# Kernel tuning notes

Measured on AMD Instinct MI355X. Metric: run time of the kernel, lower is better.

## Reference

```python
import jax, jax.numpy as jnp
import numpy as np

B, C, H, W = 2, 128, 64, 64


def setup_inputs() -> dict:
    key = jax.random.key(0)
    ks = jax.random.split(key, 16)
    s = 1.0 / np.sqrt(C)
    d = {
        "x": jax.random.normal(ks[0], (B, C, H, W), jnp.float32),
        "y": jax.random.normal(ks[1], (B, C, H, W), jnp.float32),
    }
    names = ["qr", "qi", "kr", "ki", "vr", "vi"]
    for i, n in enumerate(names):
        d["W" + n] = jax.random.normal(ks[2 + 2 * i], (C, C), jnp.float32) * s
        d["b" + n] = jax.random.normal(ks[3 + 2 * i], (C,), jnp.float32) * s
    return d


def _lin(t, Wt, bt):
    # t: [b, n, c]; torch Linear: t @ W^T + b
    return jnp.einsum("bnc,dc->bnd", t, Wt) + bt


def reference(x, y, Wqr, bqr, Wqi, bqi, Wkr, bkr, Wki, bki, Wvr, bvr, Wvi, bvi):
    b, c, h, w = x.shape
    xf = jnp.fft.fft2(x)  # over last two axes (h, w)
    yf = jnp.fft.fft2(y)
    # b c h w -> b (h w) c
    def flat(t):
        return t.transpose(0, 2, 3, 1).reshape(b, h * w, c)
    xr, xi = flat(xf.real), flat(xf.imag)
    yr, yi = flat(yf.real), flat(yf.imag)

    Qr = _lin(xr, Wqr, bqr) - _lin(xi, Wqi, bqi)
    Qi = _lin(xi, Wqr, bqr) + _lin(xr, Wqi, bqi)
    Kr = _lin(yr, Wkr, bkr) - _lin(yi, Wki, bki)
    Ki = _lin(yi, Wkr, bkr) + _lin(yr, Wki, bki)
    Vr = _lin(yr, Wvr, bvr) - _lin(yi, Wvi, bvi)
    Vi = _lin(yi, Wvr, bvr) + _lin(yr, Wvi, bvi)

    sr = jnp.einsum("bnc,bmc->bnm", Qr, Kr) - jnp.einsum("bnc,bmc->bnm", Qi, Ki)
    si = jnp.einsum("bnc,bmc->bnm", Qr, Ki) + jnp.einsum("bnc,bmc->bnm", Qi, Kr)
    scores = jnp.sqrt(sr * sr + si * si + 1e-8)
    attn = jax.nn.softmax(scores, axis=-1)

    out_r = jnp.einsum("bnm,bmc->bnc", attn, Vr)
    out_i = jnp.einsum("bnm,bmc->bnc", attn, Vi)
    out_c = jax.lax.complex(out_r, out_i)
    # b (h w) c -> b c h w
    out_c = out_c.reshape(b, h, w, c).transpose(0, 3, 1, 2)
    return jnp.fft.ifft2(out_c).real
```

## Files before the change

kernel.cpp:

```cpp
#include <hip/hip_runtime.h>
#include <math.h>


#define PI2 6.283185307179586f

typedef __attribute__((ext_vector_type(8))) short short8;
typedef __attribute__((ext_vector_type(4))) float f32x4;

#define MFMA16(A,B,C) __builtin_amdgcn_mfma_f32_16x16x32_bf16((A),(B),(C),0,0,0)

__device__ inline unsigned short f2bf(float x){
  union{float f; unsigned int u;} a; a.f = x;
  unsigned int r = (a.u + 0x7fffu + ((a.u>>16)&1u)) >> 16;
  return (unsigned short)r;
}
__device__ inline float bf2f(unsigned short h){
  union{unsigned int u; float f;} a; a.u = ((unsigned int)h)<<16; return a.f;
}
__device__ inline short8 neg8(short8 x){
  union{short8 v; unsigned int u[4];} a; a.v = x;
  a.u[0]^=0x80008000u; a.u[1]^=0x80008000u; a.u[2]^=0x80008000u; a.u[3]^=0x80008000u;
  return a.v;
}
__device__ inline void gload_lds16(const void* g, void* lds){
  __builtin_amdgcn_global_load_lds((const __attribute__((address_space(1))) unsigned int*)g,
                                   (__attribute__((address_space(3))) unsigned int*)lds,
                                   16, 0, 0);
}

__global__ __launch_bounds__(256) void dft2_fwd_kernel(
    const float* __restrict__ x, const float* __restrict__ y,
    float* __restrict__ xr, float* __restrict__ xi,
    float* __restrict__ yr, float* __restrict__ yi)
{
  __shared__ float Xs[4096];
  __shared__ float Tr[4096], Ti[4096];
  __shared__ float twc[64], tws[64];
  int blk = blockIdx.x;
  const float* src; float *outr, *outi;
  int plane;
  if (blk < 256) { src = x; outr = xr; outi = xi; plane = blk; }
  else           { src = y; outr = yr; outi = yi; plane = blk - 256; }
  int b = plane >> 7, c = plane & 127;
  int t = threadIdx.x;
  if (t < 64) {
    float ang = -PI2 * (float)t / 64.0f;
    twc[t] = cosf(ang); tws[t] = sinf(ang);
  }
  const float* p = src + ((size_t)plane << 12);
  for (int i = t; i < 4096; i += 256) Xs[i] = p[i];
  __syncthreads();
  for (int j = 0; j < 16; j++) {
    int o = t + 256 * j; int h = o >> 6, wp = o & 63;
    float ar = 0.f, ai = 0.f;
    for (int w = 0; w < 64; w++) {
      int k = (w * wp) & 63;
      float v = Xs[h * 64 + w];
      ar = fmaf(v, twc[k], ar);
      ai = fmaf(v, tws[k], ai);
    }
    Tr[h * 64 + wp] = ar; Ti[h * 64 + wp] = ai;
  }
  __syncthreads();
  size_t ob = ((size_t)b * 4096) * 128 + c;
  for (int j = 0; j < 16; j++) {
    int o = t + 256 * j; int hp = o >> 6, wp = o & 63;
    float ar = 0.f, ai = 0.f;
    for (int h = 0; h < 64; h++) {
      int k = (h * hp) & 63;
      float cr = twc[k], ci = tws[k];
      float tr = Tr[h * 64 + wp], ti = Ti[h * 64 + wp];
      ar += tr * cr - ti * ci;
      ai += tr * ci + ti * cr;
    }
    int n = (hp << 6) + wp;
    outr[ob + (size_t)n * 128] = ar;
    outi[ob + (size_t)n * 128] = ai;
  }
}

__global__ __launch_bounds__(256) void proj_pack_kernel(
    const float* __restrict__ xr, const float* __restrict__ xi,
    const float* __restrict__ yr, const float* __restrict__ yi,
    const float* __restrict__ Wqr, const float* __restrict__ bqr,
    const float* __restrict__ Wqi, const float* __restrict__ bqi,
    const float* __restrict__ Wkr, const float* __restrict__ bkr,
    const float* __restrict__ Wki, const float* __restrict__ bki,
    const float* __restrict__ Wvr, const float* __restrict__ bvr,
    const float* __restrict__ Wvi, const float* __restrict__ bvi,
    unsigned short* __restrict__ Qpk, unsigned short* __restrict__ Kpk,
    unsigned short* __restrict__ Vpk)
{
  __shared__ float Asr[64 * 33], Asi[64 * 33], Wsr[128 * 33], Wsi[128 * 33];
  int nt = blockIdx.x, lin = blockIdx.y, b = blockIdx.z;
  const float *ar, *ai, *Wr, *Wi, *br_, *bi_;
  if (lin == 0)      { ar = xr; ai = xi; Wr = Wqr; Wi = Wqi; br_ = bqr; bi_ = bqi; }
  else if (lin == 1) { ar = yr; ai = yi; Wr = Wkr; Wi = Wki; br_ = bkr; bi_ = bki; }
  else               { ar = yr; ai = yi; Wr = Wvr; Wi = Wvi; br_ = bvr; bi_ = bvi; }
  int t = threadIdx.x; int td = t & 15, tn = t >> 4;
  int n0 = nt * 64;
  size_t abase = (size_t)b * 4096 * 128 + (size_t)n0 * 128;
  float accr[4][8] = {}, acci[4][8] = {};
  for (int kk = 0; kk < 4; kk++) {
    __syncthreads();
    for (int idx = t; idx < 64 * 32; idx += 256) {
      int r = idx >> 5, ccol = idx & 31;
      Asr[r * 33 + ccol] = ar[abase + (size_t)r * 128 + kk * 32 + ccol];
      Asi[r * 33 + ccol] = ai[abase + (size_t)r * 128 + kk * 32 + ccol];
    }
    for (int idx = t; idx < 128 * 32; idx += 256) {
      int r = idx >> 5, ccol = idx & 31;
      Wsr[r * 33 + ccol] = Wr[(size_t)r * 128 + kk * 32 + ccol];
      Wsi[r * 33 + ccol] = Wi[(size_t)r * 128 + kk * 32 + ccol];
    }
    __syncthreads();
    for (int k = 0; k < 32; k++) {
      float a_r[4], a_i[4], w_r[8], w_i[8];
      #pragma unroll
      for (int i = 0; i < 4; i++) {
        a_r[i] = Asr[(tn * 4 + i) * 33 + k];
        a_i[i] = Asi[(tn * 4 + i) * 33 + k];
      }
      #pragma unroll
      for (int jj = 0; jj < 8; jj++) {
        w_r[jj] = Wsr[(td + 16 * jj) * 33 + k];
        w_i[jj] = Wsi[(td + 16 * jj) * 33 + k];
      }
      #pragma unroll
      for (int i = 0; i < 4; i++)
        #pragma unroll
        for (int jj = 0; jj < 8; jj++) {
          accr[i][jj] += a_r[i] * w_r[jj] - a_i[i] * w_i[jj];
          acci[i][jj] += a_i[i] * w_r[jj] + a_r[i] * w_i[jj];
        }
    }
  }
  for (int jj = 0; jj < 8; jj++) {
    int d = td + 16 * jj;
    float brd = br_[d], bid = bi_[d];
    #pragma unroll
    for (int i = 0; i < 4; i++) {
      int n = n0 + tn * 4 + i;
      float cr = accr[i][jj] + (brd - bid);
      float ci = acci[i][jj] + (brd + bid);
      if (lin <= 1) {
        unsigned short rh = f2bf(cr); unsigned short rl = f2bf(cr - bf2f(rh));
        unsigned short ih = f2bf(ci); unsigned short il = f2bf(ci - bf2f(ih));
        int s = d >> 5, j = d & 7;
        int lq = ((d & 31) >> 3) * 16 + (n & 15);
        if (lin == 0) {
          int tqi = n >> 4;
          size_t base = ((size_t)((b * 256 + tqi) * 16 + s)) * 512 + (size_t)lq * 8 + j;
          Qpk[base + 0 * 2048] = rh; Qpk[base + 1 * 2048] = rl;
          Qpk[base + 2 * 2048] = ih; Qpk[base + 3 * 2048] = il;
        } else {
          int mt2 = n >> 6, tml = (n >> 4) & 3;
          size_t base = ((size_t)((b * 64 + mt2) * 64 + tml * 4 + s)) * 512 + (size_t)lq * 8 + j;
          Kpk[base + 0 * 8192] = rh; Kpk[base + 1 * 8192] = rl;
          Kpk[base + 2 * 8192] = ih; Kpk[base + 3 * 8192] = il;
        }
      } else {
        int sm = n >> 5, jv = n & 7;
        int lv = ((n & 31) >> 3) * 16 + (d & 15);
        size_t b0 = ((size_t)((b * 128 + sm) * 16 + (d >> 4))) * 512 + (size_t)lv * 8 + jv;
        size_t b1 = ((size_t)((b * 128 + sm) * 16 + ((d + 128) >> 4))) * 512 + (size_t)lv * 8 + jv;
        Vpk[b0] = f2bf(cr);
        Vpk[b1] = f2bf(ci);
      }
    }
  }
}

__global__ __launch_bounds__(256, 1) void attn_mfma_kernel(
    const short* __restrict__ Qpk, const short* __restrict__ Kpk,
    const short* __restrict__ Vpk,
    float* __restrict__ Or_, float* __restrict__ Oi_)
{
  __shared__ __align__(16) short Klds[2][32768];
  __shared__ __align__(16) short Pfrag[4 * 512];
  __shared__ float rmax[2][16][2];
  __shared__ float rsum[2][16][2];

  const int b = blockIdx.y, qt = blockIdx.x;
  const int t = threadIdx.x;
  const int w = t >> 6, l = t & 63;
  const int qg = w & 1, mh = w >> 1;
  const int g = l >> 4, c = l & 15;

  const short8* Qp8 = (const short8*)Qpk;
  const int tq = qt * 2 + qg;
  short8 Qf[4][4];
  #pragma unroll
  for (int a = 0; a < 4; a++)
    #pragma unroll
    for (int s = 0; s < 4; s++)
      Qf[a][s] = Qp8[((size_t)((b * 256 + tq) * 16 + a * 4 + s)) * 64 + l];
  short8 nQih[4], nQil[4];
  #pragma unroll
  for (int s = 0; s < 4; s++) { nQih[s] = neg8(Qf[2][s]); nQil[s] = neg8(Qf[3][s]); }

  f32x4 O[8], M, L;
  #pragma unroll
  for (int nt = 0; nt < 8; nt++) O[nt] = (f32x4){0.f, 0.f, 0.f, 0.f};
  M = (f32x4){-3e38f, -3e38f, -3e38f, -3e38f};
  L = (f32x4){0.f, 0.f, 0.f, 0.f};

  const char* Kg = (const char*)Kpk;
  {
    const char* gsrc = Kg + ((size_t)(b * 64) << 16);
    char* lb = (char*)&Klds[0][0];
    #pragma unroll
    for (int i2 = 0; i2 < 16; i2++) {
      int ch = i2 * 4 + w;
      gload_lds16(gsrc + ch * 1024 + l * 16, lb + ch * 1024);
    }
  }
  const short8* Vp8 = (const short8*)Vpk;

  for (int mt = 0; mt < 64; mt++) {
    const int cur = mt & 1;
    __syncthreads();
    if (mt + 1 < 64) {
      const char* gsrc = Kg + ((size_t)(b * 64 + mt + 1) << 16);
      char* lb = (char*)&Klds[cur ^ 1][0];
      #pragma unroll
      for (int i2 = 0; i2 < 16; i2++) {
        int ch = i2 * 4 + w;
        gload_lds16(gsrc + ch * 1024 + l * 16, lb + ch * 1024);
      }
    }
    const short8* kb8 = (const short8*)&Klds[cur][0];
    f32x4 sr[2], si[2];
    #pragma unroll
    for (int tm = 0; tm < 2; tm++) { sr[tm] = (f32x4){0,0,0,0}; si[tm] = (f32x4){0,0,0,0}; }
    #pragma unroll
    for (int s = 0; s < 4; s++) {
      #pragma unroll
      for (int tm = 0; tm < 2; tm++) {
        const int tml = 2 * mh + tm;
        short8 Brh = kb8[((0 * 4 + tml) * 4 + s) * 64 + l];
        short8 Brl = kb8[((1 * 4 + tml) * 4 + s) * 64 + l];
        short8 Bih = kb8[((2 * 4 + tml) * 4 + s) * 64 + l];
        short8 Bil = kb8[((3 * 4 + tml) * 4 + s) * 64 + l];
        sr[tm] = MFMA16(Qf[0][s], Brh, sr[tm]);
        si[tm] = MFMA16(Qf[0][s], Bih, si[tm]);
        sr[tm] = MFMA16(Qf[0][s], Brl, sr[tm]);
        si[tm] = MFMA16(Qf[0][s], Bil, si[tm]);
        sr[tm] = MFMA16(Qf[1][s], Brh, sr[tm]);
        si[tm] = MFMA16(Qf[1][s], Bih, si[tm]);
        sr[tm] = MFMA16(nQih[s], Bih, sr[tm]);
        si[tm] = MFMA16(Qf[2][s], Brh, si[tm]);
        sr[tm] = MFMA16(nQih[s], Bil, sr[tm]);
        si[tm] = MFMA16(Qf[2][s], Brl, si[tm]);
        sr[tm] = MFMA16(nQil[s], Bih, sr[tm]);
        si[tm] = MFMA16(Qf[3][s], Brh, si[tm]);
      }
    }
    f32x4 s0, s1, mx;
    #pragma unroll
    for (int r = 0; r < 4; r++) {
      s0[r] = sqrtf(sr[0][r] * sr[0][r] + si[0][r] * si[0][r] + 1e-8f);
      s1[r] = sqrtf(sr[1][r] * sr[1][r] + si[1][r] * si[1][r] + 1e-8f);
      mx[r] = fmaxf(s0[r], s1[r]);
    }
    #pragma unroll
    for (int d = 1; d < 16; d <<= 1) {
      #pragma unroll
      for (int r = 0; r < 4; r++) mx[r] = fmaxf(mx[r], __shfl_xor(mx[r], d));
    }
    if (c < 4) rmax[qg][4 * g + c][mh] = mx[c];
    __syncthreads();
    f32x4 nm, esc, p0, p1, ps;
    #pragma unroll
    for (int r = 0; r < 4; r++) {
      float v = fmaxf(rmax[qg][4 * g + r][0], rmax[qg][4 * g + r][1]);
      nm[r] = fmaxf(M[r], v);
      esc[r] = __expf(M[r] - nm[r]);
      M[r] = nm[r];
      p0[r] = __expf(s0[r] - nm[r]);
      p1[r] = __expf(s1[r] - nm[r]);
      ps[r] = p0[r] + p1[r];
    }
    #pragma unroll
    for (int d = 1; d < 16; d <<= 1) {
      #pragma unroll
      for (int r = 0; r < 4; r++) ps[r] += __shfl_xor(ps[r], d);
    }
    if (c < 4) rsum[qg][4 * g + c][mh] = ps[c];
    #pragma unroll
    for (int tm = 0; tm < 2; tm++) {
      int mm = 16 * tm + c;
      int lpb = (mm >> 3) * 16;
      int j = mm & 7;
      #pragma unroll
      for (int r = 0; r < 4; r++) {
        float p = (tm == 0) ? p0[r] : p1[r];
        Pfrag[(qg * 2 + mh) * 512 + (lpb + 4 * g + r) * 8 + j] = (short)f2bf(p);
      }
    }
    __syncthreads();
    #pragma unroll
    for (int r = 0; r < 4; r++) {
      L[r] = L[r] * esc[r] + rsum[qg][4 * g + r][0] + rsum[qg][4 * g + r][1];
      #pragma unroll
      for (int nt = 0; nt < 8; nt++) O[nt][r] *= esc[r];
    }
    #pragma unroll
    for (int ks = 0; ks < 2; ks++) {
      short8 Pa = *(const short8*)&Pfrag[(qg * 2 + ks) * 512 + l * 8];
      const size_t vb = ((size_t)((b * 128 + mt * 2 + ks) * 16 + mh * 8)) * 64 + l;
      #pragma unroll
      for (int nt = 0; nt < 8; nt++) {
        short8 Vb = Vp8[vb + (size_t)nt * 64];
        O[nt] = MFMA16(Pa, Vb, O[nt]);
      }
    }
  }
  const size_t base = (size_t)b * 4096 * 128;
  f32x4 inv;
  #pragma unroll
  for (int r = 0; r < 4; r++) inv[r] = 1.0f / L[r];
  #pragma unroll
  for (int nt = 0; nt < 8; nt++) {
    int cc = mh * 128 + nt * 16 + c;
    #pragma unroll
    for (int r = 0; r < 4; r++) {
      int row = qt * 32 + qg * 16 + 4 * g + r;
      float v = O[nt][r] * inv[r];
      if (cc < 128) Or_[base + (size_t)row * 128 + cc] = v;
      else          Oi_[base + (size_t)row * 128 + cc - 128] = v;
    }
  }
}

__global__ __launch_bounds__(256) void idft2_kernel(
    const float* __restrict__ Or_, const float* __restrict__ Oi_,
    float* __restrict__ out)
{
  __shared__ float Ar[4096], Ai[4096], Tr[4096], Ti[4096];
  __shared__ float twc[64], tws[64];
  int plane = blockIdx.x; int b = plane >> 7, c = plane & 127;
  int t = threadIdx.x;
  if (t < 64) {
    float ang = PI2 * (float)t / 64.0f;
    twc[t] = cosf(ang); tws[t] = sinf(ang);
  }
  size_t ibase = (size_t)b * 4096 * 128 + c;
  for (int i = t; i < 4096; i += 256) {
    Ar[i] = Or_[ibase + (size_t)i * 128];
    Ai[i] = Oi_[ibase + (size_t)i * 128];
  }
  __syncthreads();
  for (int j = 0; j < 16; j++) {
    int o = t + 256 * j; int hp = o >> 6, w = o & 63;
    float tr = 0.f, ti = 0.f;
    for (int wp = 0; wp < 64; wp++) {
      int k = (wp * w) & 63;
      float cr = twc[k], ci = tws[k];
      float ar = Ar[hp * 64 + wp], ai = Ai[hp * 64 + wp];
      tr += ar * cr - ai * ci;
      ti += ai * cr + ar * ci;
    }
    Tr[hp * 64 + w] = tr; Ti[hp * 64 + w] = ti;
  }
  __syncthreads();
  size_t obase = ((size_t)plane) << 12;
  for (int j = 0; j < 16; j++) {
    int o = t + 256 * j; int h = o >> 6, w = o & 63;
    float acc = 0.f;
    for (int hp = 0; hp < 64; hp++) {
      int k = (hp * h) & 63;
      acc += Tr[hp * 64 + w] * twc[k] - Ti[hp * 64 + w] * tws[k];
    }
    out[obase + o] = acc * (1.0f / 4096.0f);
  }
}

extern "C" void kernel_launch(void* const* d_in, const int* in_sizes, int n_in,
                              void* d_out, int out_size, void* d_ws, size_t ws_size,
                              hipStream_t stream) {
  const float* x   = (const float*)d_in[0];
  const float* y   = (const float*)d_in[1];
  const float* Wqr = (const float*)d_in[2];  const float* bqr = (const float*)d_in[3];
  const float* Wqi = (const float*)d_in[4];  const float* bqi = (const float*)d_in[5];
  const float* Wkr = (const float*)d_in[6];  const float* bkr = (const float*)d_in[7];
  const float* Wki = (const float*)d_in[8];  const float* bki = (const float*)d_in[9];
  const float* Wvr = (const float*)d_in[10]; const float* bvr = (const float*)d_in[11];
  const float* Wvi = (const float*)d_in[12]; const float* bvi = (const float*)d_in[13];
  char* wsb = (char*)d_ws;
  if (ws_size < ((size_t)36 << 20)) return;
  unsigned short* Qpk = (unsigned short*)(wsb);
  unsigned short* Kpk = (unsigned short*)(wsb + ((size_t)8 << 20));
  unsigned short* Vpk = (unsigned short*)(wsb + ((size_t)16 << 20));
  float* xr = (float*)(wsb + ((size_t)20 << 20));
  float* xi = (float*)(wsb + ((size_t)24 << 20));
  float* yr = (float*)(wsb + ((size_t)28 << 20));
  float* yi = (float*)(wsb + ((size_t)32 << 20));
  float* Or_ = (float*)(wsb + ((size_t)20 << 20));
  float* Oi_ = (float*)(wsb + ((size_t)24 << 20));
  float* out = (float*)d_out;

  hipLaunchKernelGGL(dft2_fwd_kernel, dim3(512), dim3(256), 0, stream,
                     x, y, xr, xi, yr, yi);
  hipLaunchKernelGGL(proj_pack_kernel, dim3(64, 3, 2), dim3(256), 0, stream,
                     xr, xi, yr, yi,
                     Wqr, bqr, Wqi, bqi, Wkr, bkr, Wki, bki, Wvr, bvr, Wvi, bvi,
                     Qpk, Kpk, Vpk);
  hipLaunchKernelGGL(attn_mfma_kernel, dim3(128, 2), dim3(256), 0, stream,
                     (const short*)Qpk, (const short*)Kpk, (const short*)Vpk, Or_, Oi_);
  hipLaunchKernelGGL(idft2_kernel, dim3(256), dim3(256), 0, stream,
                     Or_, Oi_, out);
}
```

Measured before the change: 492.6 us.

## Stage packed QKV writes through LDS and split attention across eight waves

The projection kernel now writes its bf16-packed Q/K/V fragments into shared memory first, then copies them out with coalesced 16-byte global stores instead of scattered 2-byte stores. The attention kernel goes from 4 to 8 waves per block, so each wave computes one 16-key tile and half as many output columns, which halves per-wave accumulator registers. The block index is remapped so that batches interleave. Sign handling moves from precomputed negated Q fragments to negating K fragments in the inner loop. This adds per-iteration negation work and a four-way max/sum reduction through shared memory in exchange for more parallel waves and better store coalescing.

```diff
diff --git a/kernel.cpp b/kernel.cpp
--- a/kernel.cpp
+++ b/kernel.cpp
@@ -91,7 +91,13 @@
     unsigned short* __restrict__ Qpk, unsigned short* __restrict__ Kpk,
     unsigned short* __restrict__ Vpk)
 {
-  __shared__ float Asr[64 * 33], Asi[64 * 33], Wsr[128 * 33], Wsi[128 * 33];
+  __shared__ __align__(16) char smem[65536];
+  float* Asr = (float*)smem;
+  float* Asi = Asr + 64 * 33;
+  float* Wsr = Asi + 64 * 33;
+  float* Wsi = Wsr + 128 * 33;
+  unsigned short* pk = (unsigned short*)smem;
+
   int nt = blockIdx.x, lin = blockIdx.y, b = blockIdx.z;
   const float *ar, *ai, *Wr, *Wi, *br_, *bi_;
   if (lin == 0)      { ar = xr; ai = xi; Wr = Wqr; Wi = Wqi; br_ = bqr; bi_ = bqi; }
@@ -135,6 +141,7 @@
         }
     }
   }
+  __syncthreads();
   for (int jj = 0; jj < 8; jj++) {
     int d = td + 16 * jj;
     float brd = br_[d], bid = bi_[d];
@@ -148,40 +155,73 @@
         unsigned short ih = f2bf(ci); unsigned short il = f2bf(ci - bf2f(ih));
         int s = d >> 5, j = d & 7;
         int lq = ((d & 31) >> 3) * 16 + (n & 15);
+        int gi = (n >> 4) & 3;
         if (lin == 0) {
-          int tqi = n >> 4;
-          size_t base = ((size_t)((b * 256 + tqi) * 16 + s)) * 512 + (size_t)lq * 8 + j;
-          Qpk[base + 0 * 2048] = rh; Qpk[base + 1 * 2048] = rl;
-          Qpk[base + 2 * 2048] = ih; Qpk[base + 3 * 2048] = il;
+          pk[(((gi * 4 + 0) * 4 + s) * 512) + lq * 8 + j] = rh;
+          pk[(((gi * 4 + 1) * 4 + s) * 512) + lq * 8 + j] = rl;
+          pk[(((gi * 4 + 2) * 4 + s) * 512) + lq * 8 + j] = ih;
+          pk[(((gi * 4 + 3) * 4 + s) * 512) + lq * 8 + j] = il;
         } else {
-          int mt2 = n >> 6, tml = (n >> 4) & 3;
-          size_t base = ((size_t)((b * 64 + mt2) * 64 + tml * 4 + s)) * 512 + (size_t)lq * 8 + j;
-          Kpk[base + 0 * 8192] = rh; Kpk[base + 1 * 8192] = rl;
-          Kpk[base + 2 * 8192] = ih; Kpk[base + 3 * 8192] = il;
+          pk[(((0 * 4 + gi) * 4 + s) * 512) + lq * 8 + j] = rh;
+          pk[(((1 * 4 + gi) * 4 + s) * 512) + lq * 8 + j] = rl;
+          pk[(((2 * 4 + gi) * 4 + s) * 512) + lq * 8 + j] = ih;
+          pk[(((3 * 4 + gi) * 4 + s) * 512) + lq * 8 + j] = il;
         }
       } else {
-        int sm = n >> 5, jv = n & 7;
+        int smi = (n >> 5) & 1, jv = n & 7;
         int lv = ((n & 31) >> 3) * 16 + (d & 15);
-        size_t b0 = ((size_t)((b * 128 + sm) * 16 + (d >> 4))) * 512 + (size_t)lv * 8 + jv;
-        size_t b1 = ((size_t)((b * 128 + sm) * 16 + ((d + 128) >> 4))) * 512 + (size_t)lv * 8 + jv;
-        Vpk[b0] = f2bf(cr);
-        Vpk[b1] = f2bf(ci);
+        pk[(smi * 16 + (d >> 4)) * 512 + lv * 8 + jv] = f2bf(cr);
+        pk[(smi * 16 + 8 + (d >> 4)) * 512 + lv * 8 + jv] = f2bf(ci);
       }
     }
   }
-}
-
-__global__ __launch_bounds__(256, 1) void attn_mfma_kernel(
+  __syncthreads();
+  if (lin == 0) {
+    int tq0 = nt * 4;
+    #pragma unroll
+    for (int ch = 0; ch < 16; ch++) {
+      int idx = t + 256 * ch;
+      int l = idx & 63; int rest = idx >> 6;
+      int s = rest & 3, a = (rest >> 2) & 3, gi = rest >> 4;
+      short8 v = *(const short8*)(pk + (size_t)idx * 8);
+      size_t gaddr = ((size_t)((b * 256 + tq0 + gi) * 16 + a * 4 + s)) * 512 + (size_t)l * 8;
+      *(short8*)(Qpk + gaddr) = v;
+    }
+  } else if (lin == 1) {
+    int mt2 = n0 >> 6;
+    size_t gbase = ((size_t)(b * 64 + mt2)) * 32768;
+    #pragma unroll
+    for (int ch = 0; ch < 16; ch++) {
+      int idx = t + 256 * ch;
+      short8 v = *(const short8*)(pk + (size_t)idx * 8);
+      *(short8*)(Kpk + gbase + (size_t)idx * 8) = v;
+    }
+  } else {
+    int sm0 = n0 >> 5;
+    size_t gbase = ((size_t)(b * 128 + sm0)) * 8192;
+    #pragma unroll
+    for (int ch = 0; ch < 8; ch++) {
+      int idx = t + 256 * ch;
+      short8 v = *(const short8*)(pk + (size_t)idx * 8);
+      *(short8*)(Vpk + gbase + (size_t)idx * 8) = v;
+    }
+  }
+}
+
+__global__ __launch_bounds__(512, 1) void attn_mfma_kernel(
     const short* __restrict__ Qpk, const short* __restrict__ Kpk,
     const short* __restrict__ Vpk,
     float* __restrict__ Or_, float* __restrict__ Oi_)
 {
   __shared__ __align__(16) short Klds[2][32768];
   __shared__ __align__(16) short Pfrag[4 * 512];
-  __shared__ float rmax[2][16][2];
-  __shared__ float rsum[2][16][2];
-
-  const int b = blockIdx.y, qt = blockIdx.x;
+  __shared__ float rmax[2][16][4];
+  __shared__ float rsum[2][16][4];
+
+  const int bi = blockIdx.x;
+  const int xg = bi & 7;
+  const int b = xg >> 2;
+  const int qt = (bi >> 3) * 4 + (xg & 3);
   const int t = threadIdx.x;
   const int w = t >> 6, l = t & 63;
   const int qg = w & 1, mh = w >> 1;
@@ -195,13 +235,10 @@
     #pragma unroll
     for (int s = 0; s < 4; s++)
       Qf[a][s] = Qp8[((size_t)((b * 256 + tq) * 16 + a * 4 + s)) * 64 + l];
-  short8 nQih[4], nQil[4];
+
+  f32x4 O[4], M, L;
   #pragma unroll
-  for (int s = 0; s < 4; s++) { nQih[s] = neg8(Qf[2][s]); nQil[s] = neg8(Qf[3][s]); }
-
-  f32x4 O[8], M, L;
-  #pragma unroll
-  for (int nt = 0; nt < 8; nt++) O[nt] = (f32x4){0.f, 0.f, 0.f, 0.f};
+  for (int nt = 0; nt < 4; nt++) O[nt] = (f32x4){0.f, 0.f, 0.f, 0.f};
   M = (f32x4){-3e38f, -3e38f, -3e38f, -3e38f};
   L = (f32x4){0.f, 0.f, 0.f, 0.f};
 
@@ -210,8 +247,8 @@
     const char* gsrc = Kg + ((size_t)(b * 64) << 16);
     char* lb = (char*)&Klds[0][0];
     #pragma unroll
-    for (int i2 = 0; i2 < 16; i2++) {
-      int ch = i2 * 4 + w;
+    for (int i2 = 0; i2 < 8; i2++) {
+      int ch = i2 * 8 + w;
       gload_lds16(gsrc + ch * 1024 + l * 16, lb + ch * 1024);
     }
   }
@@ -224,44 +261,38 @@
       const char* gsrc = Kg + ((size_t)(b * 64 + mt + 1) << 16);
       char* lb = (char*)&Klds[cur ^ 1][0];
       #pragma unroll
-      for (int i2 = 0; i2 < 16; i2++) {
-        int ch = i2 * 4 + w;
+      for (int i2 = 0; i2 < 8; i2++) {
+        int ch = i2 * 8 + w;
         gload_lds16(gsrc + ch * 1024 + l * 16, lb + ch * 1024);
       }
     }
     const short8* kb8 = (const short8*)&Klds[cur][0];
-    f32x4 sr[2], si[2];
-    #pragma unroll
-    for (int tm = 0; tm < 2; tm++) { sr[tm] = (f32x4){0,0,0,0}; si[tm] = (f32x4){0,0,0,0}; }
+    f32x4 sr = (f32x4){0,0,0,0}, si = (f32x4){0,0,0,0};
     #pragma unroll
     for (int s = 0; s < 4; s++) {
-      #pragma unroll
-      for (int tm = 0; tm < 2; tm++) {
-        const int tml = 2 * mh + tm;
-        short8 Brh = kb8[((0 * 4 + tml) * 4 + s) * 64 + l];
-        short8 Brl = kb8[((1 * 4 + tml) * 4 + s) * 64 + l];
-        short8 Bih = kb8[((2 * 4 + tml) * 4 + s) * 64 + l];
-        short8 Bil = kb8[((3 * 4 + tml) * 4 + s) * 64 + l];
-        sr[tm] = MFMA16(Qf[0][s], Brh, sr[tm]);
-        si[tm] = MFMA16(Qf[0][s], Bih, si[tm]);
-        sr[tm] = MFMA16(Qf[0][s], Brl, sr[tm]);
-        si[tm] = MFMA16(Qf[0][s], Bil, si[tm]);
-        sr[tm] = MFMA16(Qf[1][s], Brh, sr[tm]);
-        si[tm] = MFMA16(Qf[1][s], Bih, si[tm]);
-        sr[tm] = MFMA16(nQih[s], Bih, sr[tm]);
-        si[tm] = MFMA16(Qf[2][s], Brh, si[tm]);
-        sr[tm] = MFMA16(nQih[s], Bil, sr[tm]);
-        si[tm] = MFMA16(Qf[2][s], Brl, si[tm]);
-        sr[tm] = MFMA16(nQil[s], Bih, sr[tm]);
-        si[tm] = MFMA16(Qf[3][s], Brh, si[tm]);
-      }
-    }
-    f32x4 s0, s1, mx;
+      short8 Brh = kb8[((0 * 4 + mh) * 4 + s) * 64 + l];
+      short8 Brl = kb8[((1 * 4 + mh) * 4 + s) * 64 + l];
+      short8 Bih = kb8[((2 * 4 + mh) * 4 + s) * 64 + l];
+      short8 Bil = kb8[((3 * 4 + mh) * 4 + s) * 64 + l];
+      short8 nBih = neg8(Bih), nBil = neg8(Bil);
+      sr = MFMA16(Qf[0][s], Brh, sr);
+      si = MFMA16(Qf[0][s], Bih, si);
+      sr = MFMA16(Qf[1][s], Brh, sr);
+      si = MFMA16(Qf[1][s], Bih, si);
+      sr = MFMA16(Qf[0][s], Brl, sr);
+      si = MFMA16(Qf[0][s], Bil, si);
+      sr = MFMA16(Qf[2][s], nBih, sr);
+      si = MFMA16(Qf[2][s], Brh, si);
+      sr = MFMA16(Qf[3][s], nBih, sr);
+      si = MFMA16(Qf[3][s], Brh, si);
+      sr = MFMA16(Qf[2][s], nBil, sr);
+      si = MFMA16(Qf[2][s], Brl, si);
+    }
+    f32x4 s0, mx;
     #pragma unroll
     for (int r = 0; r < 4; r++) {
-      s0[r] = sqrtf(sr[0][r] * sr[0][r] + si[0][r] * si[0][r] + 1e-8f);
-      s1[r] = sqrtf(sr[1][r] * sr[1][r] + si[1][r] * si[1][r] + 1e-8f);
-      mx[r] = fmaxf(s0[r], s1[r]);
+      s0[r] = sqrtf(sr[r] * sr[r] + si[r] * si[r] + 1e-8f);
+      mx[r] = s0[r];
     }
     #pragma unroll
     for (int d = 1; d < 16; d <<= 1) {
@@ -270,16 +301,16 @@
     }
     if (c < 4) rmax[qg][4 * g + c][mh] = mx[c];
     __syncthreads();
-    f32x4 nm, esc, p0, p1, ps;
+    f32x4 nm, esc, p, ps;
     #pragma unroll
     for (int r = 0; r < 4; r++) {
-      float v = fmaxf(rmax[qg][4 * g + r][0], rmax[qg][4 * g + r][1]);
+      float v = fmaxf(fmaxf(rmax[qg][4 * g + r][0], rmax[qg][4 * g + r][1]),
+                      fmaxf(rmax[qg][4 * g + r][2], rmax[qg][4 * g + r][3]));
       nm[r] = fmaxf(M[r], v);
       esc[r] = __expf(M[r] - nm[r]);
       M[r] = nm[r];
-      p0[r] = __expf(s0[r] - nm[r]);
-      p1[r] = __expf(s1[r] - nm[r]);
-      ps[r] = p0[r] + p1[r];
+      p[r] = __expf(s0[r] - nm[r]);
+      ps[r] = p[r];
     }
     #pragma unroll
     for (int d = 1; d < 16; d <<= 1) {
@@ -287,30 +318,28 @@
       for (int r = 0; r < 4; r++) ps[r] += __shfl_xor(ps[r], d);
     }
     if (c < 4) rsum[qg][4 * g + c][mh] = ps[c];
-    #pragma unroll
-    for (int tm = 0; tm < 2; tm++) {
-      int mm = 16 * tm + c;
-      int lpb = (mm >> 3) * 16;
-      int j = mm & 7;
-      #pragma unroll
-      for (int r = 0; r < 4; r++) {
-        float p = (tm == 0) ? p0[r] : p1[r];
-        Pfrag[(qg * 2 + mh) * 512 + (lpb + 4 * g + r) * 8 + j] = (short)f2bf(p);
-      }
+    {
+      int ks = mh >> 1;
+      int lb2 = ((mh & 1) * 2 + (c >> 3)) * 16;
+      int j = c & 7;
+      #pragma unroll
+      for (int r = 0; r < 4; r++)
+        Pfrag[(qg * 2 + ks) * 512 + (lb2 + 4 * g + r) * 8 + j] = (short)f2bf(p[r]);
     }
     __syncthreads();
     #pragma unroll
     for (int r = 0; r < 4; r++) {
-      L[r] = L[r] * esc[r] + rsum[qg][4 * g + r][0] + rsum[qg][4 * g + r][1];
-      #pragma unroll
-      for (int nt = 0; nt < 8; nt++) O[nt][r] *= esc[r];
+      L[r] = L[r] * esc[r] + rsum[qg][4 * g + r][0] + rsum[qg][4 * g + r][1]
+                           + rsum[qg][4 * g + r][2] + rsum[qg][4 * g + r][3];
+      #pragma unroll
+      for (int nt = 0; nt < 4; nt++) O[nt][r] *= esc[r];
     }
     #pragma unroll
     for (int ks = 0; ks < 2; ks++) {
       short8 Pa = *(const short8*)&Pfrag[(qg * 2 + ks) * 512 + l * 8];
-      const size_t vb = ((size_t)((b * 128 + mt * 2 + ks) * 16 + mh * 8)) * 64 + l;
-      #pragma unroll
-      for (int nt = 0; nt < 8; nt++) {
+      const size_t vb = ((size_t)((b * 128 + mt * 2 + ks) * 16 + mh * 4)) * 64 + l;
+      #pragma unroll
+      for (int nt = 0; nt < 4; nt++) {
         short8 Vb = Vp8[vb + (size_t)nt * 64];
         O[nt] = MFMA16(Pa, Vb, O[nt]);
       }
@@ -321,8 +350,8 @@
   #pragma unroll
   for (int r = 0; r < 4; r++) inv[r] = 1.0f / L[r];
   #pragma unroll
-  for (int nt = 0; nt < 8; nt++) {
-    int cc = mh * 128 + nt * 16 + c;
+  for (int nt = 0; nt < 4; nt++) {
+    int cc = mh * 64 + nt * 16 + c;
     #pragma unroll
     for (int r = 0; r < 4; r++) {
       int row = qt * 32 + qg * 16 + 4 * g + r;
@@ -406,7 +435,7 @@
                      xr, xi, yr, yi,
                      Wqr, bqr, Wqi, bqi, Wkr, bkr, Wki, bki, Wvr, bvr, Wvi, bvi,
                      Qpk, Kpk, Vpk);
-  hipLaunchKernelGGL(attn_mfma_kernel, dim3(128, 2), dim3(256), 0, stream,
+  hipLaunchKernelGGL(attn_mfma_kernel, dim3(256), dim3(512), 0, stream,
                      (const short*)Qpk, (const short*)Kpk, (const short*)Vpk, Or_, Oi_);
   hipLaunchKernelGGL(idft2_kernel, dim3(256), dim3(256), 0, stream,
                      Or_, Oi_, out);
```

New measurement: 480.0 us. 2.6% less time.
